# Kernel optimization log

Hardware: AMD Instinct MI355X
Metric: run time of the kernel (lower is better)

Reference implementation:

```python
import jax, jax.numpy as jnp
import numpy as np

B, N, D_IN = 2, 2048, 2048
D_OUT, H, KV = 2048, 32, 8
G = H // KV          # group_size = 4
DH = D_OUT // H      # head dim = 64


def setup_inputs() -> dict:
    key = jax.random.key(0)
    k0, k1, k2, k3, k4, k5 = jax.random.split(key, 6)
    s_in = 1.0 / np.sqrt(D_IN)
    s_out = 1.0 / np.sqrt(D_OUT)
    return {
        "x": jax.random.normal(k0, (B, N, D_IN), dtype=jnp.float32),
        "Wq": jax.random.normal(k1, (D_IN, H * DH), dtype=jnp.float32) * s_in,
        "Wk": jax.random.normal(k2, (D_IN, KV * DH), dtype=jnp.float32) * s_in,
        "Wv": jax.random.normal(k3, (D_IN, KV * DH), dtype=jnp.float32) * s_in,
        "Wo": jax.random.normal(k4, (D_OUT, D_IN), dtype=jnp.float32) * s_out,
        "bo": jax.random.normal(k5, (D_IN,), dtype=jnp.float32) * 0.01,
    }


def gqa_forward(x, Wq, Wk, Wv, Wo, bo):
    b, n, _ = x.shape
    scale = 1.0 / jnp.sqrt(jnp.asarray(DH, x.dtype))
    # projections
    q = (x @ Wq).reshape(b, n, KV, G, DH)   # queries grouped by shared kv head
    k = (x @ Wk).reshape(b, n, KV, DH)
    v = (x @ Wv).reshape(b, n, KV, DH)
    # scores: (B, KV, G, N, N) — equivalent to repeat_interleave of K over groups
    scores = jnp.einsum('bnkgd,bmkd->bkgnm', q, k) * scale
    causal = jnp.triu(jnp.ones((n, n), dtype=bool), k=1)
    scores = jnp.where(causal, -jnp.inf, scores)
    attn = jax.nn.softmax(scores, axis=-1)
    # dropout p=0.0 -> identity
    ctx = jnp.einsum('bkgnm,bmkd->bnkgd', attn, v).reshape(b, n, D_OUT)
    return ctx @ Wo + bo


def reference(x, Wq, Wk, Wv, Wo, bo):
    return gqa_forward(x, Wq, Wk, Wv, Wo, bo)
```

## Files before the change

kernel.cpp:

```cpp
#include <hip/hip_runtime.h>
#include <hip/hip_bf16.h>
#include <cstdint>


#define B_    2
#define N_    2048
#define DIN_  2048
#define H_    32
#define KV_   8
#define DH_   64
#define M_    4096
#define NQKV_ 3072

typedef float f32x4 __attribute__((ext_vector_type(4)));
typedef __bf16 bf16x8 __attribute__((ext_vector_type(8)));
typedef unsigned short u16x8 __attribute__((ext_vector_type(8)));

__device__ __forceinline__ unsigned short f32_to_bf16_bits(float f) {
  unsigned int u = __float_as_uint(f);
  u = (u + 0x7FFFu + ((u >> 16) & 1u)) >> 16;
  return (unsigned short)u;
}

__device__ __forceinline__ void gload_lds16(const void* g, void* l) {
  __builtin_amdgcn_global_load_lds(
      (__attribute__((address_space(1))) void*)(g),
      (__attribute__((address_space(3))) void*)(l), 16, 0, 0);
}

__global__ __launch_bounds__(256) void prep(
    const float* __restrict__ x, const float* __restrict__ Wq,
    const float* __restrict__ Wk, const float* __restrict__ Wv,
    const float* __restrict__ Wo,
    unsigned short* __restrict__ Xb, unsigned short* __restrict__ Wqkv,
    unsigned short* __restrict__ Wot, float qscale) {
  const int task = blockIdx.y, tid = threadIdx.x;
  if (task == 0) {
    size_t i0 = ((size_t)blockIdx.x * 256 + tid) * 2;
#pragma unroll
    for (int t = 0; t < 2; ++t) {
      float4 v = ((const float4*)x)[i0 + t];
      ushort4 o;
      o.x = f32_to_bf16_bits(v.x);
      o.y = f32_to_bf16_bits(v.y);
      o.z = f32_to_bf16_bits(v.z);
      o.w = f32_to_bf16_bits(v.w);
      ((ushort4*)Xb)[i0 + t] = o;
    }
    return;
  }
  const float* src;
  unsigned short* dst;
  int NC, off;
  float scale = 1.0f;
  switch (task) {
    case 1: src = Wq; dst = Wqkv; NC = 2048; off = 0;    scale = qscale; break;
    case 2: src = Wk; dst = Wqkv; NC = 512;  off = 2048; break;
    case 3: src = Wv; dst = Wqkv; NC = 512;  off = 2560; break;
    default: src = Wo; dst = Wot; NC = 2048; off = 0;    break;
  }
  const int nx = NC >> 5;
  const int bx = blockIdx.x;
  if (bx >= nx * 64) return;
  const int n0 = (bx % nx) * 32, k0 = (bx / nx) * 32;
  __shared__ float tile[32][33];
  const int tx = tid & 31, ty = tid >> 5;
#pragma unroll
  for (int i = 0; i < 32; i += 8)
    tile[ty + i][tx] = src[(size_t)(k0 + ty + i) * NC + n0 + tx];
  __syncthreads();
#pragma unroll
  for (int i = 0; i < 32; i += 8)
    dst[(size_t)(off + n0 + ty + i) * 2048 + k0 + tx] =
        f32_to_bf16_bits(tile[tx][ty + i] * scale);
}

__global__ __launch_bounds__(256) void transpose_v(
    const unsigned short* __restrict__ QKV, unsigned short* __restrict__ Vtg) {
  __shared__ unsigned short t[64][72];
  int nt = blockIdx.x, bkv = blockIdx.y;
  int b = bkv >> 3, kv = bkv & 7;
  int tid = threadIdx.x;
  int row = tid >> 2, c = (tid & 3) * 16;
  const unsigned short* src =
      QKV + (size_t)(b * N_ + nt * 64 + row) * NQKV_ + 2560 + kv * 64;
  *(u16x8*)&t[row][c]     = *(const u16x8*)(src + c);
  *(u16x8*)&t[row][c + 8] = *(const u16x8*)(src + c + 8);
  __syncthreads();
  int d = tid >> 2;
  unsigned short* dst = Vtg + ((size_t)bkv * 64 + d) * N_ + nt * 64 + c;
  u16x8 o0, o1;
#pragma unroll
  for (int i = 0; i < 8; ++i) { o0[i] = t[c + i][d]; o1[i] = t[c + 8 + i][d]; }
  *(u16x8*)dst = o0;
  *(u16x8*)(dst + 8) = o1;
}

template <bool OUT_BF16, bool BIAS>
__global__ __launch_bounds__(256, 3) void gemm_bt(
    const unsigned short* __restrict__ A,
    const unsigned short* __restrict__ Bt,
    void* __restrict__ Cv,
    const float* __restrict__ bias,
    int Nn, int K) {
  __shared__ unsigned short As[128 * 32];
  __shared__ unsigned short Bs[128 * 32];

  const int tid = threadIdx.x;
  const int lane = tid & 63;
  const int wave = tid >> 6;
  const int wm = wave >> 1, wn = wave & 1;
  const int l16 = lane & 15, quad = lane >> 4;
  const int m0 = blockIdx.y * 128, n0 = blockIdx.x * 128;

  f32x4 acc[4][4] = {};

  const int srow = tid >> 2;
  const int kc = tid & 3;

  for (int kk = 0; kk < K; kk += 32) {
#pragma unroll
    for (int c = 0; c < 2; ++c) {
      int r = c * 64 + srow;
      int ofs = r * 32 + kc * 8;
      gload_lds16(A + (size_t)(m0 + r) * K + kk + kc * 8, (char*)As + ofs * 2);
      gload_lds16(Bt + (size_t)(n0 + r) * K + kk + kc * 8, (char*)Bs + ofs * 2);
    }
    __syncthreads();
    bf16x8 af[4], bfr[4];
#pragma unroll
    for (int mi = 0; mi < 4; ++mi)
      af[mi] = *(const bf16x8*)&As[(wm * 64 + mi * 16 + l16) * 32 + quad * 8];
#pragma unroll
    for (int ni = 0; ni < 4; ++ni)
      bfr[ni] = *(const bf16x8*)&Bs[(wn * 64 + ni * 16 + l16) * 32 + quad * 8];
#pragma unroll
    for (int mi = 0; mi < 4; ++mi)
#pragma unroll
      for (int ni = 0; ni < 4; ++ni)
        acc[mi][ni] = __builtin_amdgcn_mfma_f32_16x16x32_bf16(
            af[mi], bfr[ni], acc[mi][ni], 0, 0, 0);
    __syncthreads();
  }

  unsigned short* Cb = (unsigned short*)Cv;
  float* Cf = (float*)Cv;
#pragma unroll
  for (int mi = 0; mi < 4; ++mi) {
    int rrow = m0 + wm * 64 + mi * 16 + quad * 4;
#pragma unroll
    for (int ni = 0; ni < 4; ++ni) {
      int col = n0 + wn * 64 + ni * 16 + l16;
      float bv = BIAS ? bias[col] : 0.0f;
#pragma unroll
      for (int r = 0; r < 4; ++r) {
        float v = acc[mi][ni][r] + bv;
        if (OUT_BF16)
          Cb[(size_t)(rrow + r) * Nn + col] = f32_to_bf16_bits(v);
        else
          Cf[(size_t)(rrow + r) * Nn + col] = v;
      }
    }
  }
}

__global__ __launch_bounds__(256, 4) void attn_fwd(
    const unsigned short* __restrict__ QKV,
    const unsigned short* __restrict__ Vtg,
    unsigned short* __restrict__ Ctx) {
  __shared__ unsigned short Ks[2][64 * 64];
  __shared__ unsigned short Vs[2][64 * 64];
  __shared__ unsigned short Ps[4][16 * 64];

  const int p = blockIdx.x;
  const int h = blockIdx.y, b = blockIdx.z;
  const int kv = h >> 2;
  const int tid = threadIdx.x, lane = tid & 63, wave = tid >> 6;
  const int l16 = lane & 15, quad = lane >> 4;
  const size_t baserow = (size_t)b * N_;
  const unsigned short* Kg = QKV + 2048 + kv * 64;
  const unsigned short* Vg = Vtg + (size_t)(b * KV_ + kv) * 64 * N_;
  const int sw = l16 & 7;
  unsigned short* Pw = &Ps[wave][0];

  auto stageKV = [&](int j, int buf) {
#pragma unroll
    for (int it = 0; it < 2; ++it) {
      int c = tid + it * 256;
      int row = c >> 3, off = ((c & 7) ^ (row & 7)) * 8;
      gload_lds16(Kg + (baserow + j * 64 + row) * NQKV_ + off,
                  (char*)Ks[buf] + c * 16);
      gload_lds16(Vg + (size_t)row * N_ + j * 64 + off,
                  (char*)Vs[buf] + c * 16);
    }
  };

#pragma unroll 1
  for (int phase = 0; phase < 2; ++phase) {
    const int qtile = phase ? p : 31 - p;
    const int q0 = qtile * 64;

    bf16x8 qa[2];
#pragma unroll
    for (int ks = 0; ks < 2; ++ks)
      qa[ks] = *(const bf16x8*)(QKV +
          (baserow + q0 + wave * 16 + l16) * NQKV_ + h * 64 + ks * 32 + quad * 8);

    f32x4 oacc[4] = {};
    float lp[4] = {0.f, 0.f, 0.f, 0.f};

    __syncthreads();
    stageKV(0, 0);

    for (int j = 0; j <= qtile; ++j) {
      __syncthreads();
      const int buf = j & 1;
      if (j < qtile) stageKV(j + 1, buf ^ 1);

      f32x4 sc[4] = {};
#pragma unroll
      for (int ks = 0; ks < 2; ++ks)
#pragma unroll
        for (int ni = 0; ni < 4; ++ni) {
          bf16x8 kb = *(const bf16x8*)&Ks[buf][(ni * 16 + l16) * 64 +
                                              ((ks * 4 + quad) ^ sw) * 8];
          sc[ni] = __builtin_amdgcn_mfma_f32_16x16x32_bf16(qa[ks], kb, sc[ni], 0, 0, 0);
        }

      if (j == qtile) {
        const int qrow = q0 + wave * 16 + quad * 4;
#pragma unroll
        for (int ni = 0; ni < 4; ++ni) {
          int kcol = q0 + ni * 16 + l16;
#pragma unroll
          for (int r = 0; r < 4; ++r)
            if (kcol > qrow + r) sc[ni][r] = -1e30f;
        }
      }
#pragma unroll
      for (int ni = 0; ni < 4; ++ni) {
        const int cl = ni * 2 + (l16 >> 3);
#pragma unroll
        for (int r = 0; r < 4; ++r) {
          float pe = __builtin_amdgcn_exp2f(sc[ni][r]);
          lp[r] += pe;
          int row = quad * 4 + r;
          Pw[row * 64 + ((cl ^ (row & 7)) * 8) + (l16 & 7)] =
              (unsigned short)(__float_as_uint(pe) >> 16);
        }
      }
      bf16x8 pa[2];
#pragma unroll
      for (int ks = 0; ks < 2; ++ks)
        pa[ks] = *(const bf16x8*)&Pw[l16 * 64 + ((ks * 4 + quad) ^ sw) * 8];
#pragma unroll
      for (int ks = 0; ks < 2; ++ks)
#pragma unroll
        for (int di = 0; di < 4; ++di) {
          bf16x8 vb = *(const bf16x8*)&Vs[buf][(di * 16 + l16) * 64 +
                                              ((ks * 4 + quad) ^ sw) * 8];
          oacc[di] = __builtin_amdgcn_mfma_f32_16x16x32_bf16(pa[ks], vb, oacc[di], 0, 0, 0);
        }
    }

    float inv[4];
#pragma unroll
    for (int r = 0; r < 4; ++r) {
      float v = lp[r];
#pragma unroll
      for (int off = 1; off < 16; off <<= 1) v += __shfl_xor(v, off);
      inv[r] = 1.0f / v;
    }
#pragma unroll
    for (int di = 0; di < 4; ++di)
#pragma unroll
      for (int r = 0; r < 4; ++r) {
        size_t row = baserow + q0 + wave * 16 + quad * 4 + r;
        Ctx[row * 2048 + h * 64 + di * 16 + l16] =
            f32_to_bf16_bits(oacc[di][r] * inv[r]);
      }
  }
}

extern "C" void kernel_launch(void* const* d_in, const int* in_sizes, int n_in,
                              void* d_out, int out_size, void* d_ws, size_t ws_size,
                              hipStream_t stream) {
  const float* x  = (const float*)d_in[0];
  const float* Wq = (const float*)d_in[1];
  const float* Wk = (const float*)d_in[2];
  const float* Wv = (const float*)d_in[3];
  const float* Wo = (const float*)d_in[4];
  const float* bo = (const float*)d_in[5];
  float* out = (float*)d_out;

  unsigned short* Xb   = (unsigned short*)d_ws;
  unsigned short* Wqkv = Xb + (size_t)M_ * DIN_;
  unsigned short* QKV  = Wqkv + (size_t)NQKV_ * DIN_;
  unsigned short* Wot  = QKV + (size_t)M_ * NQKV_;
  unsigned short* Ctx  = Xb;
  unsigned short* Vtg  = Wqkv;

  const float kQScale = 0.125f * 1.44269504088896340736f;

  prep<<<dim3(4096, 5), 256, 0, stream>>>(x, Wq, Wk, Wv, Wo, Xb, Wqkv, Wot, kQScale);

  gemm_bt<true, false><<<dim3(NQKV_ / 128, M_ / 128), 256, 0, stream>>>(
      Xb, Wqkv, QKV, nullptr, NQKV_, DIN_);

  transpose_v<<<dim3(N_ / 64, B_ * KV_), 256, 0, stream>>>(QKV, Vtg);

  attn_fwd<<<dim3(16, 32, 2), 256, 0, stream>>>(QKV, Vtg, Ctx);

  gemm_bt<false, true><<<dim3(DIN_ / 128, M_ / 128), 256, 0, stream>>>(
      Ctx, Wot, out, bo, DIN_, 2048);
}
```

Baseline: 290.9 us.

## Share K/V tiles across all four GQA heads within one attention block

Restructures the attention kernel so each block handles one KV head, with each of its four waves computing one query head over all 64 query rows of the tile. K/V tiles staged in LDS are reused by the four heads, and K/V fragments are loaded into registers once per iteration, which cuts global K/V traffic and LDS reads by a factor of four. In exchange the grid shrinks to 256 blocks with launch bounds of 1, so fewer waves are resident per CU, register pressure rises with 16 accumulators per wave, and LDS usage for P grows.

```diff
diff --git a/kernel.cpp b/kernel.cpp
--- a/kernel.cpp
+++ b/kernel.cpp
@@ -164,24 +164,23 @@
   }
 }
 
-__global__ __launch_bounds__(256, 4) void attn_fwd(
+__global__ __launch_bounds__(256, 1) void attn_fwd(
     const unsigned short* __restrict__ QKV,
     const unsigned short* __restrict__ Vtg,
     unsigned short* __restrict__ Ctx) {
   __shared__ unsigned short Ks[2][64 * 64];
   __shared__ unsigned short Vs[2][64 * 64];
-  __shared__ unsigned short Ps[4][16 * 64];
+  __shared__ unsigned short Ps[4][4][16 * 64];
 
   const int p = blockIdx.x;
-  const int h = blockIdx.y, b = blockIdx.z;
-  const int kv = h >> 2;
+  const int kv = blockIdx.y, b = blockIdx.z;
   const int tid = threadIdx.x, lane = tid & 63, wave = tid >> 6;
   const int l16 = lane & 15, quad = lane >> 4;
+  const int h = kv * 4 + wave;
   const size_t baserow = (size_t)b * N_;
   const unsigned short* Kg = QKV + 2048 + kv * 64;
   const unsigned short* Vg = Vtg + (size_t)(b * KV_ + kv) * 64 * N_;
   const int sw = l16 & 7;
-  unsigned short* Pw = &Ps[wave][0];
 
   auto stageKV = [&](int j, int buf) {
 #pragma unroll
@@ -200,14 +199,16 @@
     const int qtile = phase ? p : 31 - p;
     const int q0 = qtile * 64;
 
-    bf16x8 qa[2];
-#pragma unroll
-    for (int ks = 0; ks < 2; ++ks)
-      qa[ks] = *(const bf16x8*)(QKV +
-          (baserow + q0 + wave * 16 + l16) * NQKV_ + h * 64 + ks * 32 + quad * 8);
-
-    f32x4 oacc[4] = {};
-    float lp[4] = {0.f, 0.f, 0.f, 0.f};
+    bf16x8 qa[4][2];
+#pragma unroll
+    for (int s = 0; s < 4; ++s)
+#pragma unroll
+      for (int ks = 0; ks < 2; ++ks)
+        qa[s][ks] = *(const bf16x8*)(QKV +
+            (baserow + q0 + s * 16 + l16) * NQKV_ + h * 64 + ks * 32 + quad * 8);
+
+    f32x4 oacc[4][4] = {};
+    float lp[4][4] = {};
 
     __syncthreads();
     stageKV(0, 0);
@@ -217,68 +218,89 @@
       const int buf = j & 1;
       if (j < qtile) stageKV(j + 1, buf ^ 1);
 
-      f32x4 sc[4] = {};
+      bf16x8 kb[2][4];
 #pragma unroll
       for (int ks = 0; ks < 2; ++ks)
 #pragma unroll
+        for (int ni = 0; ni < 4; ++ni)
+          kb[ks][ni] = *(const bf16x8*)&Ks[buf][(ni * 16 + l16) * 64 +
+                                               ((ks * 4 + quad) ^ sw) * 8];
+
+#pragma unroll
+      for (int s = 0; s < 4; ++s) {
+        f32x4 sc[4] = {};
+#pragma unroll
+        for (int ks = 0; ks < 2; ++ks)
+#pragma unroll
+          for (int ni = 0; ni < 4; ++ni)
+            sc[ni] = __builtin_amdgcn_mfma_f32_16x16x32_bf16(
+                qa[s][ks], kb[ks][ni], sc[ni], 0, 0, 0);
+        if (j == qtile) {
+          const int qrow = q0 + s * 16 + quad * 4;
+#pragma unroll
+          for (int ni = 0; ni < 4; ++ni) {
+            int kcol = q0 + ni * 16 + l16;
+#pragma unroll
+            for (int r = 0; r < 4; ++r)
+              if (kcol > qrow + r) sc[ni][r] = -1e30f;
+          }
+        }
+        unsigned short* Pw = &Ps[wave][s][0];
+#pragma unroll
         for (int ni = 0; ni < 4; ++ni) {
-          bf16x8 kb = *(const bf16x8*)&Ks[buf][(ni * 16 + l16) * 64 +
-                                              ((ks * 4 + quad) ^ sw) * 8];
-          sc[ni] = __builtin_amdgcn_mfma_f32_16x16x32_bf16(qa[ks], kb, sc[ni], 0, 0, 0);
-        }
-
-      if (j == qtile) {
-        const int qrow = q0 + wave * 16 + quad * 4;
-#pragma unroll
-        for (int ni = 0; ni < 4; ++ni) {
-          int kcol = q0 + ni * 16 + l16;
-#pragma unroll
-          for (int r = 0; r < 4; ++r)
-            if (kcol > qrow + r) sc[ni][r] = -1e30f;
+          const int cl = ni * 2 + (l16 >> 3);
+#pragma unroll
+          for (int r = 0; r < 4; ++r) {
+            float pe = __builtin_amdgcn_exp2f(sc[ni][r]);
+            lp[s][r] += pe;
+            int row = quad * 4 + r;
+            Pw[row * 64 + ((cl ^ (row & 7)) * 8) + (l16 & 7)] =
+                (unsigned short)(__float_as_uint(pe) >> 16);
+          }
         }
       }
-#pragma unroll
-      for (int ni = 0; ni < 4; ++ni) {
-        const int cl = ni * 2 + (l16 >> 3);
+
+      bf16x8 vb[2][4];
+#pragma unroll
+      for (int ks = 0; ks < 2; ++ks)
+#pragma unroll
+        for (int di = 0; di < 4; ++di)
+          vb[ks][di] = *(const bf16x8*)&Vs[buf][(di * 16 + l16) * 64 +
+                                               ((ks * 4 + quad) ^ sw) * 8];
+#pragma unroll
+      for (int s = 0; s < 4; ++s) {
+        bf16x8 pa[2];
+#pragma unroll
+        for (int ks = 0; ks < 2; ++ks)
+          pa[ks] = *(const bf16x8*)&Ps[wave][s][l16 * 64 + ((ks * 4 + quad) ^ sw) * 8];
+#pragma unroll
+        for (int ks = 0; ks < 2; ++ks)
+#pragma unroll
+          for (int di = 0; di < 4; ++di)
+            oacc[s][di] = __builtin_amdgcn_mfma_f32_16x16x32_bf16(
+                pa[ks], vb[ks][di], oacc[s][di], 0, 0, 0);
+      }
+    }
+
+#pragma unroll
+    for (int s = 0; s < 4; ++s) {
+      float inv[4];
+#pragma unroll
+      for (int r = 0; r < 4; ++r) {
+        float v = lp[s][r];
+#pragma unroll
+        for (int off = 1; off < 16; off <<= 1) v += __shfl_xor(v, off);
+        inv[r] = 1.0f / v;
+      }
+#pragma unroll
+      for (int di = 0; di < 4; ++di)
 #pragma unroll
         for (int r = 0; r < 4; ++r) {
-          float pe = __builtin_amdgcn_exp2f(sc[ni][r]);
-          lp[r] += pe;
-          int row = quad * 4 + r;
-          Pw[row * 64 + ((cl ^ (row & 7)) * 8) + (l16 & 7)] =
-              (unsigned short)(__float_as_uint(pe) >> 16);
+          size_t row = baserow + q0 + s * 16 + quad * 4 + r;
+          Ctx[row * 2048 + h * 64 + di * 16 + l16] =
+              f32_to_bf16_bits(oacc[s][di][r] * inv[r]);
         }
-      }
-      bf16x8 pa[2];
-#pragma unroll
-      for (int ks = 0; ks < 2; ++ks)
-        pa[ks] = *(const bf16x8*)&Pw[l16 * 64 + ((ks * 4 + quad) ^ sw) * 8];
-#pragma unroll
-      for (int ks = 0; ks < 2; ++ks)
-#pragma unroll
-        for (int di = 0; di < 4; ++di) {
-          bf16x8 vb = *(const bf16x8*)&Vs[buf][(di * 16 + l16) * 64 +
-                                              ((ks * 4 + quad) ^ sw) * 8];
-          oacc[di] = __builtin_amdgcn_mfma_f32_16x16x32_bf16(pa[ks], vb, oacc[di], 0, 0, 0);
-        }
-    }
-
-    float inv[4];
-#pragma unroll
-    for (int r = 0; r < 4; ++r) {
-      float v = lp[r];
-#pragma unroll
-      for (int off = 1; off < 16; off <<= 1) v += __shfl_xor(v, off);
-      inv[r] = 1.0f / v;
-    }
-#pragma unroll
-    for (int di = 0; di < 4; ++di)
-#pragma unroll
-      for (int r = 0; r < 4; ++r) {
-        size_t row = baserow + q0 + wave * 16 + quad * 4 + r;
-        Ctx[row * 2048 + h * 64 + di * 16 + l16] =
-            f32_to_bf16_bits(oacc[di][r] * inv[r]);
-      }
+    }
   }
 }
 
@@ -309,7 +331,7 @@
 
   transpose_v<<<dim3(N_ / 64, B_ * KV_), 256, 0, stream>>>(QKV, Vtg);
 
-  attn_fwd<<<dim3(16, 32, 2), 256, 0, stream>>>(QKV, Vtg, Ctx);
+  attn_fwd<<<dim3(16, 8, 2), 256, 0, stream>>>(QKV, Vtg, Ctx);
 
   gemm_bt<false, true><<<dim3(DIN_ / 128, M_ / 128), 256, 0, stream>>>(
       Ctx, Wot, out, bo, DIN_, 2048);
```

Measured after the change: 307.3 us. +5.6%, slower.
